# Optimization experiments

Measured on AMD Instinct MI355X. Metric: run time of the kernel, lower is better.

Reference implementation:

```python
import jax, jax.numpy as jnp
import numpy as np

V, BLOCK, L, H, C = 50257, 1024, 4, 12, 768
HS = C // H  # 64
EPS = 1e-6  # flax LayerNorm default


def _ln(x, scale, bias):
    mu = jnp.mean(x, axis=-1, keepdims=True)
    var = jnp.var(x, axis=-1, keepdims=True)
    return (x - mu) * jax.lax.rsqrt(var + EPS) * scale + bias


def setup_inputs() -> dict:
    key = jax.random.key(0)
    ks = jax.random.split(key, 12)
    B, T = 2, 1024
    inp = {
        'idx': jax.random.randint(ks[0], (B, T), 0, V),
        'targets': jax.random.randint(ks[1], (B, T), 0, V),
        'wte': jax.random.normal(ks[2], (V, C), jnp.float32) * 0.02,
        'wpe': jax.random.normal(ks[3], (BLOCK, C), jnp.float32) * 0.02,
        'ln1_s': jnp.ones((L, C), jnp.float32),
        'ln1_b': jnp.zeros((L, C), jnp.float32),
        'attn_k': jax.random.normal(ks[4], (L, C, H, 3 * HS), jnp.float32) * 0.02,
        'attn_b': jnp.zeros((L, H, 3 * HS), jnp.float32),
        'aproj_k': jax.random.normal(ks[5], (L, C, C), jnp.float32) * 0.02,
        'aproj_b': jnp.zeros((L, C), jnp.float32),
        'ln2_s': jnp.ones((L, C), jnp.float32),
        'ln2_b': jnp.zeros((L, C), jnp.float32),
        'fc_k': jax.random.normal(ks[6], (L, C, 4 * C), jnp.float32) * 0.02,
        'fc_b': jnp.zeros((L, 4 * C), jnp.float32),
        'mproj_k': jax.random.normal(ks[7], (L, 4 * C, C), jnp.float32) * 0.02,
        'mproj_b': jnp.zeros((L, C), jnp.float32),
        'lnf_s': jnp.ones((C,), jnp.float32),
        'lnf_b': jnp.zeros((C,), jnp.float32),
    }
    return inp


def _block(x, ln1_s, ln1_b, Wqkv, bqkv, Wo, bo, ln2_s, ln2_b, Wfc, bfc, Wmp, bmp, mask):
    B, T, _ = x.shape
    h = _ln(x, ln1_s, ln1_b)
    qkv = jnp.einsum('btc,chd->bhtd', h, Wqkv) + bqkv[:, None, :]  # [B,H,T,3HS]
    q, k, v = jnp.split(qkv, 3, axis=-1)
    att = jnp.einsum('bhtd,bhsd->bhts', q, k) * (1.0 / jnp.sqrt(jnp.float32(HS)))
    att = jnp.where(mask, att, -jnp.inf)
    att = jax.nn.softmax(att, axis=-1)
    y = jnp.einsum('bhts,bhsd->bthd', att, v).reshape(B, T, C)
    x = x + y @ Wo + bo
    h = _ln(x, ln2_s, ln2_b)
    h = jax.nn.gelu(h @ Wfc + bfc, approximate=True)
    x = x + h @ Wmp + bmp
    return x


def reference(idx, targets, wte, wpe, ln1_s, ln1_b, attn_k, attn_b, aproj_k, aproj_b,
              ln2_s, ln2_b, fc_k, fc_b, mproj_k, mproj_b, lnf_s, lnf_b):
    B, T = idx.shape
    x = wte[idx] + wpe[jnp.arange(T)][None]  # [B,T,C]
    mask = jnp.tril(jnp.ones((T, T), bool))[None, None]
    for l in range(L):
        x = _block(x, ln1_s[l], ln1_b[l], attn_k[l], attn_b[l], aproj_k[l], aproj_b[l],
                   ln2_s[l], ln2_b[l], fc_k[l], fc_b[l], mproj_k[l], mproj_b[l], mask)
    x = _ln(x, lnf_s, lnf_b)
    logits = jnp.einsum('btc,vc->btv', x, wte)  # tied output projection (wte.attend)
    logp = jax.nn.log_softmax(logits, axis=-1)
    loss = -jnp.mean(jnp.take_along_axis(logp, targets[..., None], axis=-1))
    return logits, loss
```

## Files before the change

kernel.cpp:

```cpp
#include <hip/hip_runtime.h>
#include <hip/hip_bf16.h>
#include <math.h>

typedef __attribute__((ext_vector_type(8))) short bf16x8;
typedef __attribute__((ext_vector_type(4))) float f32x4;

static constexpr int Bv   = 2;
static constexpr int Tv   = 1024;
static constexpr int Cv   = 768;
static constexpr int Hv   = 12;
static constexpr int Lv   = 4;
static constexpr int Vv   = 50257;
static constexpr int Mv   = 2048;
static constexpr int NT2  = 197;
static constexpr float EPSv = 1e-6f;

__device__ __forceinline__ void gload16(const void* g, void* l) {
    __builtin_amdgcn_global_load_lds((const __attribute__((address_space(1))) void*)g,
                                     (__attribute__((address_space(3))) void*)l, 16, 0, 0);
}
template<int N>
__device__ __forceinline__ void waitvm_barrier() {
    if constexpr (N == 0)      asm volatile("s_waitcnt vmcnt(0)\ns_barrier" ::: "memory");
    else if constexpr (N == 2) asm volatile("s_waitcnt vmcnt(2)\ns_barrier" ::: "memory");
    else if constexpr (N == 3) asm volatile("s_waitcnt vmcnt(3)\ns_barrier" ::: "memory");
    else if constexpr (N == 4) asm volatile("s_waitcnt vmcnt(4)\ns_barrier" ::: "memory");
    else if constexpr (N == 6) asm volatile("s_waitcnt vmcnt(6)\ns_barrier" ::: "memory");
    else                       asm volatile("s_waitcnt vmcnt(8)\ns_barrier" ::: "memory");
}
__device__ __forceinline__ void lgkm0_barrier() {
    asm volatile("s_waitcnt lgkmcnt(0)\ns_barrier" ::: "memory");
}

__global__ void embed_kernel(const int* __restrict__ idx,
                             const float* __restrict__ wte,
                             const float* __restrict__ wpe,
                             float* __restrict__ x) {
    int row = blockIdx.x;
    int t   = row & (Tv - 1);
    int tok = idx[row];
    const float* src = wte + (size_t)tok * Cv;
    const float* pos = wpe + (size_t)t * Cv;
    float* dst = x + (size_t)row * Cv;
    for (int c = threadIdx.x; c < Cv; c += 256)
        dst[c] = src[c] + pos[c];
}

__device__ __forceinline__ ushort4 pack4bf(float4 v) {
    ushort4 u;
    u.x = __bfloat16_as_ushort(__float2bfloat16(v.x));
    u.y = __bfloat16_as_ushort(__float2bfloat16(v.y));
    u.z = __bfloat16_as_ushort(__float2bfloat16(v.z));
    u.w = __bfloat16_as_ushort(__float2bfloat16(v.w));
    return u;
}

__global__ void ln_kernel(const float* __restrict__ in,
                          const float* __restrict__ sc,
                          const float* __restrict__ bi,
                          __hip_bfloat16* __restrict__ out) {
    int row  = blockIdx.x * 4 + (threadIdx.x >> 6);
    int lane = threadIdx.x & 63;
    const float4* xr = (const float4*)(in + (size_t)row * Cv);
    float4 a = xr[lane], b = xr[lane + 64], c = xr[lane + 128];
    float sum = a.x + a.y + a.z + a.w + b.x + b.y + b.z + b.w + c.x + c.y + c.z + c.w;
    float sq  = a.x*a.x + a.y*a.y + a.z*a.z + a.w*a.w
              + b.x*b.x + b.y*b.y + b.z*b.z + b.w*b.w
              + c.x*c.x + c.y*c.y + c.z*c.z + c.w*c.w;
    #pragma unroll
    for (int off = 32; off; off >>= 1) {
        sum += __shfl_xor(sum, off, 64);
        sq  += __shfl_xor(sq,  off, 64);
    }
    float mean = sum * (1.0f / Cv);
    float var  = sq * (1.0f / Cv) - mean * mean;
    float rs   = rsqrtf(var + EPSv);
    const float4* s4 = (const float4*)sc;
    const float4* b4 = (const float4*)bi;
    ushort4* orow = (ushort4*)(out + (size_t)row * Cv);
    #pragma unroll
    for (int i = 0; i < 3; ++i) {
        float4 v = (i == 0) ? a : (i == 1) ? b : c;
        float4 s = s4[lane + 64 * i];
        float4 t = b4[lane + 64 * i];
        float4 o;
        o.x = (v.x - mean) * rs * s.x + t.x;
        o.y = (v.y - mean) * rs * s.y + t.y;
        o.z = (v.z - mean) * rs * s.z + t.z;
        o.w = (v.w - mean) * rs * s.w + t.w;
        orow[lane + 64 * i] = pack4bf(o);
    }
}

__global__ void wtrans_kernel(const float* __restrict__ in,
                              __hip_bfloat16* __restrict__ out, int K, int N,
                              size_t inLS, size_t outLS) {
    __shared__ float tile[32][33];
    in  += (size_t)blockIdx.z * inLS;
    out += (size_t)blockIdx.z * outLS;
    int k0 = blockIdx.y * 32, n0 = blockIdx.x * 32;
    int tx = threadIdx.x & 31, ty = threadIdx.x >> 5;
    #pragma unroll
    for (int i = 0; i < 4; ++i)
        tile[ty + i * 8][tx] = in[(size_t)(k0 + ty + i * 8) * N + n0 + tx];
    __syncthreads();
    #pragma unroll
    for (int i = 0; i < 4; ++i)
        out[(size_t)(n0 + ty + i * 8) * K + k0 + tx] =
            __float2bfloat16(tile[tx][ty + i * 8]);
}

__global__ void cvt_kernel(const float* __restrict__ in,
                           __hip_bfloat16* __restrict__ out, int n4) {
    int stride = gridDim.x * 256;
    for (int i = blockIdx.x * 256 + threadIdx.x; i < n4; i += stride) {
        float4 v = ((const float4*)in)[i];
        ((ushort4*)out)[i] = pack4bf(v);
    }
}

__global__ void vtrans_kernel(const __hip_bfloat16* __restrict__ qkv,
                              __hip_bfloat16* __restrict__ vt) {
    __shared__ __hip_bfloat16 tile[32][33];
    int bh = blockIdx.z;
    int b = bh / Hv, h = bh % Hv;
    int t0 = blockIdx.x * 32, d0 = blockIdx.y * 32;
    int tx = threadIdx.x & 31, ty = threadIdx.x >> 5;
    #pragma unroll
    for (int i = 0; i < 4; ++i)
        tile[ty + i * 8][tx] =
            qkv[(size_t)(b * Tv + t0 + ty + i * 8) * 2304 + h * 192 + 128 + d0 + tx];
    __syncthreads();
    #pragma unroll
    for (int i = 0; i < 4; ++i)
        vt[((size_t)bh * 64 + d0 + ty + i * 8) * Tv + t0 + tx] = tile[tx][ty + i * 8];
}

template<int EPI, int BM>
__launch_bounds__(256)
__global__ void gemm_bf16(const __hip_bfloat16* __restrict__ A,
                          const __hip_bfloat16* __restrict__ Bt,
                          const float* __restrict__ bias,
                          const float* R, float* Cf,
                          __hip_bfloat16* __restrict__ Cb,
                          int M, int N, int K) {
    constexpr int FM  = BM / 32;
    constexpr int NA  = BM / 64;
    constexpr int LPT = NA + 1;
    __shared__ __hip_bfloat16 As[3][BM * 32];
    __shared__ __hip_bfloat16 Bs[3][64 * 32];
    int tid = threadIdx.x;
    int wave = tid >> 6, lane = tid & 63;
    int wr = wave >> 1, wc = wave & 1;
    int rowBase = blockIdx.y * BM, colBase = blockIdx.x * 64;

    f32x4 acc[FM][2] = {};

    int srow  = wave * 16 + (lane >> 2);
    int skcol = (lane & 3) * 8;
    const __hip_bfloat16* Ap0 = A + (size_t)(rowBase + srow) * K + skcol;
    const __hip_bfloat16* Ap1 = (NA > 1) ? (Ap0 + (size_t)64 * K) : Ap0;
    const __hip_bfloat16* Bp0 = Bt + (size_t)(colBase + srow) * K + skcol;
    int ldso = wave * 512;

    int aoff = (wr * (BM / 2) + (lane & 15)) * 32 + (lane >> 4) * 8;
    int boff = (wc * 32 + (lane & 15)) * 32 + (lane >> 4) * 8;

    auto stage = [&](int buf) {
        gload16(Ap0, &As[buf][ldso]);
        if constexpr (NA > 1) gload16(Ap1, &As[buf][2048 + ldso]);
        gload16(Bp0, &Bs[buf][ldso]);
        Ap0 += 32;
        if constexpr (NA > 1) Ap1 += 32;
        Bp0 += 32;
    };

    stage(0); stage(1); stage(2);

    int nt = K / 32;
    int cur = 0;
    for (int t = 0; t < nt; ++t) {
        if (t < nt - 2)       waitvm_barrier<2 * LPT>();
        else if (t == nt - 2) waitvm_barrier<LPT>();
        else                  waitvm_barrier<0>();

        bf16x8 av[FM], bv[2];
        #pragma unroll
        for (int m = 0; m < FM; ++m) av[m] = *(const bf16x8*)&As[cur][aoff + m * 512];
        #pragma unroll
        for (int n = 0; n < 2; ++n)  bv[n] = *(const bf16x8*)&Bs[cur][boff + n * 512];
        lgkm0_barrier();

        if (t + 3 < nt) stage(cur);

        #pragma unroll
        for (int m = 0; m < FM; ++m)
            #pragma unroll
            for (int n = 0; n < 2; ++n)
                acc[m][n] = __builtin_amdgcn_mfma_f32_16x16x32_bf16(
                    av[m], bv[n], acc[m][n], 0, 0, 0);
        cur = (cur == 2) ? 0 : cur + 1;
    }

    int fq = lane >> 4, fr = lane & 15;
    #pragma unroll
    for (int m = 0; m < FM; ++m) {
        #pragma unroll
        for (int n = 0; n < 2; ++n) {
            f32x4 v = acc[m][n];
            int col = colBase + wc * 32 + n * 16 + fr;
            #pragma unroll
            for (int j = 0; j < 4; ++j) {
                int row = rowBase + wr * (BM / 2) + m * 16 + fq * 4 + j;
                float val = v[j] + bias[col];
                if (EPI == 1) {
                    val += R[(size_t)row * N + col];
                    Cf[(size_t)row * N + col] = val;
                } else {
                    if (EPI == 2) {
                        float u = val;
                        float cc = 0.7978845608028654f * (u + 0.044715f * u * u * u);
                        val = 0.5f * u * (1.0f + tanhf(cc));
                    }
                    Cb[(size_t)row * N + col] = __float2bfloat16(val);
                }
            }
        }
    }
}

__launch_bounds__(256)
__global__ void attn_kernel(const __hip_bfloat16* __restrict__ qkv,
                            const __hip_bfloat16* __restrict__ vt,
                            __hip_bfloat16* __restrict__ att) {
    __shared__ __hip_bfloat16 Qs[64 * 64];
    __shared__ __hip_bfloat16 Ks[64 * 64];
    __shared__ __hip_bfloat16 Vs[64 * 64];
    __shared__ __hip_bfloat16 Ps[64 * 64];
    int bh = blockIdx.x;
    int b = bh / Hv, h = bh % Hv;
    int qt = (int)gridDim.y - 1 - (int)blockIdx.y;
    int q0 = qt * 64;
    int tid = threadIdx.x, wave = tid >> 6, lane = tid & 63;
    int g = lane >> 4, fr = lane & 15;
    int srow8 = lane >> 3, sc8 = lane & 7;

    const __hip_bfloat16* qbase = qkv + (size_t)(b * Tv + q0) * 2304 + h * 192;
    #pragma unroll
    for (int i = 0; i < 2; ++i) {
        int row = wave * 16 + i * 8 + srow8;
        gload16(qbase + (size_t)row * 2304 + ((sc8 ^ (row & 7)) * 8),
                Qs + (wave * 16 + i * 8) * 64);
    }

    f32x4 accO[4] = {};
    float mrun[4] = {-1e30f, -1e30f, -1e30f, -1e30f};
    float lrun[4] = {0.f, 0.f, 0.f, 0.f};

    for (int kv = 0; kv <= qt; ++kv) {
        int s0 = kv * 64;
        __syncthreads();
        const __hip_bfloat16* kbase = qkv + (size_t)(b * Tv + s0) * 2304 + h * 192 + 64;
        const __hip_bfloat16* vbase = vt + (size_t)bh * 64 * Tv + s0;
        #pragma unroll
        for (int i = 0; i < 2; ++i) {
            int row = wave * 16 + i * 8 + srow8;
            gload16(kbase + (size_t)row * 2304 + ((sc8 ^ (row & 7)) * 8),
                    Ks + (wave * 16 + i * 8) * 64);
            gload16(vbase + (size_t)row * Tv + ((sc8 ^ (row & 7)) * 8),
                    Vs + (wave * 16 + i * 8) * 64);
        }
        __syncthreads();

        f32x4 s4[4] = {};
        #pragma unroll
        for (int kk = 0; kk < 2; ++kk) {
            int qrow = wave * 16 + fr;
            bf16x8 qa = *(const bf16x8*)&Qs[qrow * 64 + (((g + 4 * kk) ^ (fr & 7)) * 8)];
            #pragma unroll
            for (int n = 0; n < 4; ++n) {
                int krow = n * 16 + fr;
                bf16x8 kb = *(const bf16x8*)&Ks[krow * 64 + (((g + 4 * kk) ^ (fr & 7)) * 8)];
                s4[n] = __builtin_amdgcn_mfma_f32_16x16x32_bf16(qa, kb, s4[n], 0, 0, 0);
            }
        }

        bool dia = (kv == qt);
        #pragma unroll
        for (int j = 0; j < 4; ++j) {
            int qg = q0 + wave * 16 + g * 4 + j;
            float sj[4], mx = -1e30f;
            #pragma unroll
            for (int n = 0; n < 4; ++n) {
                float v = s4[n][j] * 0.125f;
                if (dia && (s0 + n * 16 + fr) > qg) v = -1e30f;
                sj[n] = v;
                mx = fmaxf(mx, v);
            }
            #pragma unroll
            for (int off = 1; off < 16; off <<= 1)
                mx = fmaxf(mx, __shfl_xor(mx, off, 64));
            float mnew = fmaxf(mrun[j], mx);
            float ps = 0.f;
            unsigned short pb[4];
            #pragma unroll
            for (int n = 0; n < 4; ++n) {
                float p = __expf(sj[n] - mnew);
                __hip_bfloat16 pc = __float2bfloat16(p);
                pb[n] = __bfloat16_as_ushort(pc);
                ps += __bfloat162float(pc);
            }
            #pragma unroll
            for (int off = 1; off < 16; off <<= 1)
                ps += __shfl_xor(ps, off, 64);
            float cr = __expf(mrun[j] - mnew);
            lrun[j] = lrun[j] * cr + ps;
            mrun[j] = mnew;
            int prow = wave * 16 + g * 4 + j;
            #pragma unroll
            for (int n = 0; n < 4; ++n) {
                int byteoff = (32 * n + 2 * fr) ^ ((prow & 7) << 4);
                ((unsigned short*)Ps)[prow * 64 + (byteoff >> 1)] = pb[n];
            }
            #pragma unroll
            for (int n = 0; n < 4; ++n) accO[n][j] *= cr;
        }
        __syncthreads();

        #pragma unroll
        for (int kk = 0; kk < 2; ++kk) {
            int prow = wave * 16 + fr;
            bf16x8 pa = *(const bf16x8*)&Ps[prow * 64 + (((g + 4 * kk) ^ (fr & 7)) * 8)];
            #pragma unroll
            for (int n = 0; n < 4; ++n) {
                int vrow = n * 16 + fr;
                bf16x8 vb = *(const bf16x8*)&Vs[vrow * 64 + (((g + 4 * kk) ^ (fr & 7)) * 8)];
                accO[n] = __builtin_amdgcn_mfma_f32_16x16x32_bf16(pa, vb, accO[n], 0, 0, 0);
            }
        }
    }

    #pragma unroll
    for (int j = 0; j < 4; ++j) {
        float inv = 1.0f / lrun[j];
        int row = b * Tv + q0 + wave * 16 + g * 4 + j;
        #pragma unroll
        for (int n = 0; n < 4; ++n)
            att[(size_t)row * Cv + h * 64 + n * 16 + fr] =
                __float2bfloat16(accO[n][j] * inv);
    }
}

__launch_bounds__(512, 1)
__global__ void lmhead_kernel(const __hip_bfloat16* __restrict__ A,
                              const __hip_bfloat16* __restrict__ Bt,
                              float* __restrict__ Cf,
                              float* __restrict__ pLse) {
    constexpr int K = Cv, N = Vv;
    constexpr int nt = K / 64;
    __shared__ __hip_bfloat16 As[2][16384];
    __shared__ __hip_bfloat16 Bs[2][16384];
    __shared__ float ps[4][256];

    int bid = blockIdx.x;
    int nid = (bid & 7) * NT2 + (bid >> 3);
    int rowT = nid & 7, colT = nid >> 3;
    int rowBase = rowT * 256, colBase = colT * 256;

    int tid = threadIdx.x;
    int wv = tid >> 6, lane = tid & 63;
    int wr = wv >> 2, wc = wv & 3;
    int fq = lane >> 4, fr = lane & 15;
    int fr7 = fr & 7;

    f32x4 acc[8][4] = {};

    int r8 = lane >> 3;
    int cOff = ((lane & 7) ^ r8) * 8;
    const __hip_bfloat16* ApS[4];
    const __hip_bfloat16* BpS[4];
    #pragma unroll
    for (int i = 0; i < 4; ++i) {
        int rit = wv * 32 + i * 8 + r8;
        ApS[i] = A + (size_t)(rowBase + rit) * K + cOff;
        int rb = colBase + rit;
        if (rb >= N) rb = N - 1;
        BpS[i] = Bt + (size_t)rb * K + cOff;
    }

    auto stage = [&](int buf, int tile) {
        int k0 = tile * 64;
        #pragma unroll
        for (int i = 0; i < 4; ++i)
            gload16(ApS[i] + k0, &As[buf][(wv * 4 + i) * 512]);
        #pragma unroll
        for (int i = 0; i < 4; ++i)
            gload16(BpS[i] + k0, &Bs[buf][(wv * 4 + i) * 512]);
    };

    stage(0, 0);
    stage(1, 1);
    waitvm_barrier<8>();

    for (int t = 0; t < nt; ++t) {
        int cur = t & 1;
        const __hip_bfloat16* Ab = &As[cur][0];
        const __hip_bfloat16* Bb = &Bs[cur][0];

        bf16x8 av0[8], bv0[4];
        #pragma unroll
        for (int m = 0; m < 8; ++m)
            av0[m] = *(const bf16x8*)&Ab[(wr * 128 + m * 16 + fr) * 64 + ((fq ^ fr7) * 8)];
        #pragma unroll
        for (int n = 0; n < 4; ++n)
            bv0[n] = *(const bf16x8*)&Bb[(wc * 64 + n * 16 + fr) * 64 + ((fq ^ fr7) * 8)];
        __builtin_amdgcn_s_setprio(1);
        #pragma unroll
        for (int m = 0; m < 8; ++m)
            #pragma unroll
            for (int n = 0; n < 4; ++n)
                acc[m][n] = __builtin_amdgcn_mfma_f32_16x16x32_bf16(
                    av0[m], bv0[n], acc[m][n], 0, 0, 0);
        __builtin_amdgcn_s_setprio(0);

        bf16x8 av1[8], bv1[4];
        #pragma unroll
        for (int m = 0; m < 8; ++m)
            av1[m] = *(const bf16x8*)&Ab[(wr * 128 + m * 16 + fr) * 64 + (((4 + fq) ^ fr7) * 8)];
        #pragma unroll
        for (int n = 0; n < 4; ++n)
            bv1[n] = *(const bf16x8*)&Bb[(wc * 64 + n * 16 + fr) * 64 + (((4 + fq) ^ fr7) * 8)];
        lgkm0_barrier();

        if (t + 2 < nt) stage(cur, t + 2);

        __builtin_amdgcn_s_setprio(1);
        #pragma unroll
        for (int m = 0; m < 8; ++m)
            #pragma unroll
            for (int n = 0; n < 4; ++n)
                acc[m][n] = __builtin_amdgcn_mfma_f32_16x16x32_bf16(
                    av1[m], bv1[n], acc[m][n], 0, 0, 0);
        __builtin_amdgcn_s_setprio(0);

        if (t + 2 < nt) waitvm_barrier<8>();
        else            waitvm_barrier<0>();
    }

    #pragma unroll
    for (int m = 0; m < 8; ++m) {
        #pragma unroll
        for (int j = 0; j < 4; ++j) {
            int row = rowBase + wr * 128 + m * 16 + fq * 4 + j;
            float s = 0.f;
            #pragma unroll
            for (int n = 0; n < 4; ++n) {
                int col = colBase + wc * 64 + n * 16 + fr;
                float v = acc[m][n][j];
                if (col < N) {
                    Cf[(size_t)row * N + col] = v;
                    s += __expf(v);
                }
            }
            #pragma unroll
            for (int off = 1; off < 16; off <<= 1)
                s += __shfl_xor(s, off, 64);
            if (fr == 0)
                ps[wc][wr * 128 + m * 16 + fq * 4 + j] = s;
        }
    }
    __syncthreads();
    if (tid < 256)
        pLse[(size_t)(rowBase + tid) * NT2 + colT] =
            ps[0][tid] + ps[1][tid] + ps[2][tid] + ps[3][tid];
}

__global__ void plse_reduce_kernel(const float* __restrict__ pLse,
                                   const float* __restrict__ logits,
                                   const int* __restrict__ targets,
                                   float* __restrict__ rloss) {
    int row  = blockIdx.x * 4 + (threadIdx.x >> 6);
    int lane = threadIdx.x & 63;
    const float* pr = pLse + (size_t)row * NT2;
    float l = 0.f;
    for (int i = lane; i < NT2; i += 64) l += pr[i];
    #pragma unroll
    for (int off = 32; off; off >>= 1) l += __shfl_xor(l, off, 64);
    if (lane == 0)
        rloss[row] = logf(l) - logits[(size_t)row * Vv + targets[row]];
}

__global__ void loss_final_kernel(const float* __restrict__ rloss,
                                  float* __restrict__ out, int out_size) {
    float s = 0.f;
    for (int i = threadIdx.x; i < Mv; i += 256) s += rloss[i];
    #pragma unroll
    for (int off = 32; off; off >>= 1) s += __shfl_xor(s, off, 64);
    __shared__ float sw[4];
    int wave = threadIdx.x >> 6, lane = threadIdx.x & 63;
    if (lane == 0) sw[wave] = s;
    __syncthreads();
    if (threadIdx.x == 0)
        out[out_size - 1] = (sw[0] + sw[1] + sw[2] + sw[3]) / (float)Mv;
}

extern "C" void kernel_launch(void* const* d_in, const int* in_sizes, int n_in,
                              void* d_out, int out_size, void* d_ws, size_t ws_size,
                              hipStream_t stream) {
    const int*   idx     = (const int*)  d_in[0];
    const int*   targets = (const int*)  d_in[1];
    const float* wte     = (const float*)d_in[2];
    const float* wpe     = (const float*)d_in[3];
    const float* ln1_s   = (const float*)d_in[4];
    const float* ln1_b   = (const float*)d_in[5];
    const float* attn_k  = (const float*)d_in[6];
    const float* attn_b  = (const float*)d_in[7];
    const float* aproj_k = (const float*)d_in[8];
    const float* aproj_b = (const float*)d_in[9];
    const float* ln2_s   = (const float*)d_in[10];
    const float* ln2_b   = (const float*)d_in[11];
    const float* fc_k    = (const float*)d_in[12];
    const float* fc_b    = (const float*)d_in[13];
    const float* mproj_k = (const float*)d_in[14];
    const float* mproj_b = (const float*)d_in[15];
    const float* lnf_s   = (const float*)d_in[16];
    const float* lnf_b   = (const float*)d_in[17];

    float* out = (float*)d_out;
    char* ws  = (char*)d_ws;
    char* ob  = (char*)d_out;

    constexpr size_t NEED = 81962496ULL;
    if (ws_size < NEED) return;

    __hip_bfloat16* wte_bf = (__hip_bfloat16*)(ws + 0);
    __hip_bfloat16* h_bf   = (__hip_bfloat16*)(ws + 77194752);
    float*          pLse   = (float*)(ws + 80340480);
    float*          rloss  = (float*)(ws + 81954304);

    float*          x      = (float*)(ob + 0);
    __hip_bfloat16* qkv_bf = (__hip_bfloat16*)(ob + 6291456);
    __hip_bfloat16* vt_bf  = (__hip_bfloat16*)(ob + 15728640);
    __hip_bfloat16* att_bf = (__hip_bfloat16*)(ob + 18874368);
    __hip_bfloat16* fco_bf = (__hip_bfloat16*)(ob + 22020096);
    __hip_bfloat16* w0     = (__hip_bfloat16*)(ob + 34603008);
    __hip_bfloat16* w1     = (__hip_bfloat16*)(ob + 48758784);
    __hip_bfloat16* w2     = (__hip_bfloat16*)(ob + 53477376);
    __hip_bfloat16* w3     = (__hip_bfloat16*)(ob + 72351744);

    embed_kernel<<<Mv, 256, 0, stream>>>(idx, wte, wpe, x);

    wtrans_kernel<<<dim3(72, 24, 4), 256, 0, stream>>>(
        attn_k, w0, Cv, 2304, (size_t)Cv * 2304, (size_t)2304 * Cv);
    wtrans_kernel<<<dim3(24, 24, 4), 256, 0, stream>>>(
        aproj_k, w1, Cv, Cv, (size_t)Cv * Cv, (size_t)Cv * Cv);
    wtrans_kernel<<<dim3(96, 24, 4), 256, 0, stream>>>(
        fc_k, w2, Cv, 3072, (size_t)Cv * 3072, (size_t)3072 * Cv);
    wtrans_kernel<<<dim3(24, 96, 4), 256, 0, stream>>>(
        mproj_k, w3, 3072, Cv, (size_t)3072 * Cv, (size_t)Cv * 3072);

    for (int l = 0; l < Lv; ++l) {
        ln_kernel<<<512, 256, 0, stream>>>(x, ln1_s + l * Cv, ln1_b + l * Cv, h_bf);
        gemm_bf16<0, 128><<<dim3(36, 16), 256, 0, stream>>>(
            h_bf, w0 + (size_t)l * 2304 * Cv, attn_b + l * 2304, nullptr, nullptr,
            qkv_bf, Mv, 2304, Cv);
        vtrans_kernel<<<dim3(32, 2, 24), 256, 0, stream>>>(qkv_bf, vt_bf);
        attn_kernel<<<dim3(24, 16), 256, 0, stream>>>(qkv_bf, vt_bf, att_bf);
        gemm_bf16<1, 64><<<dim3(12, 32), 256, 0, stream>>>(
            att_bf, w1 + (size_t)l * Cv * Cv, aproj_b + l * Cv, x, x, nullptr,
            Mv, Cv, Cv);
        ln_kernel<<<512, 256, 0, stream>>>(x, ln2_s + l * Cv, ln2_b + l * Cv, h_bf);
        gemm_bf16<2, 128><<<dim3(48, 16), 256, 0, stream>>>(
            h_bf, w2 + (size_t)l * 3072 * Cv, fc_b + l * 3072, nullptr, nullptr,
            fco_bf, Mv, 3072, Cv);
        gemm_bf16<1, 64><<<dim3(12, 32), 256, 0, stream>>>(
            fco_bf, w3 + (size_t)l * Cv * 3072, mproj_b + l * Cv, x, x, nullptr,
            Mv, Cv, 3072);
    }

    ln_kernel<<<512, 256, 0, stream>>>(x, lnf_s, lnf_b, h_bf);
    cvt_kernel<<<2048, 256, 0, stream>>>(wte, wte_bf, (Vv * Cv) / 4);
    lmhead_kernel<<<8 * NT2, 512, 0, stream>>>(h_bf, wte_bf, out, pLse);
    plse_reduce_kernel<<<512, 256, 0, stream>>>(pLse, out, targets, rloss);
    loss_final_kernel<<<1, 256, 0, stream>>>(rloss, out, out_size);
}
```

Baseline: 942.1 us.

## Fuse V transpose into QKV GEMM epilogue and merge small launches

The QKV GEMM blocks that produce V now transpose their tile through LDS and write it straight into the vt buffer, replacing the separate vtrans kernel. The four weight-transpose launches are merged into one flat-grid kernel. The final loss reduction kernel is replaced by per-block atomicAdd into a slot zeroed inside cvt_kernel. This cuts launch count and one pass over V, but makes the loss summation order nondeterministic and skips writing V into qkv_bf.

Result: no change. 931.1 us (-1.2%).

```diff
diff --git a/kernel.cpp b/kernel.cpp
--- a/kernel.cpp
+++ b/kernel.cpp
@@ -92,13 +92,23 @@
     }
 }
 
-__global__ void wtrans_kernel(const float* __restrict__ in,
-                              __hip_bfloat16* __restrict__ out, int K, int N,
-                              size_t inLS, size_t outLS) {
+__global__ void wtrans_all_kernel(const float* __restrict__ a0, __hip_bfloat16* __restrict__ o0,
+                                  const float* __restrict__ a1, __hip_bfloat16* __restrict__ o1,
+                                  const float* __restrict__ a2, __hip_bfloat16* __restrict__ o2,
+                                  const float* __restrict__ a3, __hip_bfloat16* __restrict__ o3) {
     __shared__ float tile[32][33];
-    in  += (size_t)blockIdx.z * inLS;
-    out += (size_t)blockIdx.z * outLS;
-    int k0 = blockIdx.y * 32, n0 = blockIdx.x * 32;
+    int bid = blockIdx.x;
+    const float* in; __hip_bfloat16* out; int K, N, t;
+    if (bid < 6912)       { int l = bid / 1728;          t = bid % 1728;
+        in = a0 + (size_t)l * 768 * 2304; out = o0 + (size_t)l * 2304 * 768; K = 768;  N = 2304; }
+    else if (bid < 9216)  { int r = bid - 6912;  int l = r / 576;  t = r % 576;
+        in = a1 + (size_t)l * 768 * 768;  out = o1 + (size_t)l * 768 * 768;  K = 768;  N = 768;  }
+    else if (bid < 18432) { int r = bid - 9216;  int l = r / 2304; t = r % 2304;
+        in = a2 + (size_t)l * 768 * 3072; out = o2 + (size_t)l * 3072 * 768; K = 768;  N = 3072; }
+    else                  { int r = bid - 18432; int l = r / 2304; t = r % 2304;
+        in = a3 + (size_t)l * 3072 * 768; out = o3 + (size_t)l * 768 * 3072; K = 3072; N = 768;  }
+    int nx = N / 32;
+    int n0 = (t % nx) * 32, k0 = (t / nx) * 32;
     int tx = threadIdx.x & 31, ty = threadIdx.x >> 5;
     #pragma unroll
     for (int i = 0; i < 4; ++i)
@@ -111,29 +121,14 @@
 }
 
 __global__ void cvt_kernel(const float* __restrict__ in,
-                           __hip_bfloat16* __restrict__ out, int n4) {
+                           __hip_bfloat16* __restrict__ out, int n4,
+                           float* __restrict__ lossSlot) {
+    if (blockIdx.x == 0 && threadIdx.x == 0) *lossSlot = 0.f;
     int stride = gridDim.x * 256;
     for (int i = blockIdx.x * 256 + threadIdx.x; i < n4; i += stride) {
         float4 v = ((const float4*)in)[i];
         ((ushort4*)out)[i] = pack4bf(v);
     }
-}
-
-__global__ void vtrans_kernel(const __hip_bfloat16* __restrict__ qkv,
-                              __hip_bfloat16* __restrict__ vt) {
-    __shared__ __hip_bfloat16 tile[32][33];
-    int bh = blockIdx.z;
-    int b = bh / Hv, h = bh % Hv;
-    int t0 = blockIdx.x * 32, d0 = blockIdx.y * 32;
-    int tx = threadIdx.x & 31, ty = threadIdx.x >> 5;
-    #pragma unroll
-    for (int i = 0; i < 4; ++i)
-        tile[ty + i * 8][tx] =
-            qkv[(size_t)(b * Tv + t0 + ty + i * 8) * 2304 + h * 192 + 128 + d0 + tx];
-    __syncthreads();
-    #pragma unroll
-    for (int i = 0; i < 4; ++i)
-        vt[((size_t)bh * 64 + d0 + ty + i * 8) * Tv + t0 + tx] = tile[tx][ty + i * 8];
 }
 
 template<int EPI, int BM>
@@ -143,6 +138,7 @@
                           const float* __restrict__ bias,
                           const float* R, float* Cf,
                           __hip_bfloat16* __restrict__ Cb,
+                          __hip_bfloat16* __restrict__ vt,
                           int M, int N, int K) {
     constexpr int FM  = BM / 32;
     constexpr int NA  = BM / 64;
@@ -203,6 +199,37 @@
     }
 
     int fq = lane >> 4, fr = lane & 15;
+
+    if (EPI == 0 && vt != nullptr && (blockIdx.x % 3) == 2) {
+        __hip_bfloat16 (*Ts)[132] = (__hip_bfloat16(*)[132])&As[0][0];
+        __syncthreads();
+        #pragma unroll
+        for (int m = 0; m < FM; ++m) {
+            #pragma unroll
+            for (int n = 0; n < 2; ++n) {
+                int dloc = wc * 32 + n * 16 + fr;
+                #pragma unroll
+                for (int j = 0; j < 4; ++j) {
+                    int tl = wr * (BM / 2) + m * 16 + fq * 4 + j;
+                    float val = acc[m][n][j] + bias[colBase + dloc];
+                    Ts[dloc][tl] = __float2bfloat16(val);
+                }
+            }
+        }
+        __syncthreads();
+        int h  = blockIdx.x / 3;
+        int b  = rowBase >> 10;
+        int bh = b * Hv + h;
+        int t0 = rowBase & 1023;
+        int d = tid >> 2, part = tid & 3;
+        const ushort4* src = (const ushort4*)&Ts[d][part * 32];
+        ushort4* dst = (ushort4*)((__hip_bfloat16*)vt +
+                       ((size_t)bh * 64 + d) * Tv + t0 + part * 32);
+        #pragma unroll
+        for (int i = 0; i < 8; ++i) dst[i] = src[i];
+        return;
+    }
+
     #pragma unroll
     for (int m = 0; m < FM; ++m) {
         #pragma unroll
@@ -478,30 +505,21 @@
 __global__ void plse_reduce_kernel(const float* __restrict__ pLse,
                                    const float* __restrict__ logits,
                                    const int* __restrict__ targets,
-                                   float* __restrict__ rloss) {
-    int row  = blockIdx.x * 4 + (threadIdx.x >> 6);
+                                   float* __restrict__ lossOut) {
+    int wave = threadIdx.x >> 6;
+    int row  = blockIdx.x * 4 + wave;
     int lane = threadIdx.x & 63;
     const float* pr = pLse + (size_t)row * NT2;
     float l = 0.f;
     for (int i = lane; i < NT2; i += 64) l += pr[i];
     #pragma unroll
     for (int off = 32; off; off >>= 1) l += __shfl_xor(l, off, 64);
+    __shared__ float sr[4];
     if (lane == 0)
-        rloss[row] = logf(l) - logits[(size_t)row * Vv + targets[row]];
-}
-
-__global__ void loss_final_kernel(const float* __restrict__ rloss,
-                                  float* __restrict__ out, int out_size) {
-    float s = 0.f;
-    for (int i = threadIdx.x; i < Mv; i += 256) s += rloss[i];
-    #pragma unroll
-    for (int off = 32; off; off >>= 1) s += __shfl_xor(s, off, 64);
-    __shared__ float sw[4];
-    int wave = threadIdx.x >> 6, lane = threadIdx.x & 63;
-    if (lane == 0) sw[wave] = s;
+        sr[wave] = logf(l) - logits[(size_t)row * Vv + targets[row]];
     __syncthreads();
     if (threadIdx.x == 0)
-        out[out_size - 1] = (sw[0] + sw[1] + sw[2] + sw[3]) / (float)Mv;
+        atomicAdd(lossOut, (sr[0] + sr[1] + sr[2] + sr[3]) * (1.0f / Mv));
 }
 
 extern "C" void kernel_launch(void* const* d_in, const int* in_sizes, int n_in,
@@ -536,7 +554,6 @@
     __hip_bfloat16* wte_bf = (__hip_bfloat16*)(ws + 0);
     __hip_bfloat16* h_bf   = (__hip_bfloat16*)(ws + 77194752);
     float*          pLse   = (float*)(ws + 80340480);
-    float*          rloss  = (float*)(ws + 81954304);
 
     float*          x      = (float*)(ob + 0);
     __hip_bfloat16* qkv_bf = (__hip_bfloat16*)(ob + 6291456);
@@ -548,39 +565,33 @@
     __hip_bfloat16* w2     = (__hip_bfloat16*)(ob + 53477376);
     __hip_bfloat16* w3     = (__hip_bfloat16*)(ob + 72351744);
 
+    float* lossSlot = out + (out_size - 1);
+
     embed_kernel<<<Mv, 256, 0, stream>>>(idx, wte, wpe, x);
 
-    wtrans_kernel<<<dim3(72, 24, 4), 256, 0, stream>>>(
-        attn_k, w0, Cv, 2304, (size_t)Cv * 2304, (size_t)2304 * Cv);
-    wtrans_kernel<<<dim3(24, 24, 4), 256, 0, stream>>>(
-        aproj_k, w1, Cv, Cv, (size_t)Cv * Cv, (size_t)Cv * Cv);
-    wtrans_kernel<<<dim3(96, 24, 4), 256, 0, stream>>>(
-        fc_k, w2, Cv, 3072, (size_t)Cv * 3072, (size_t)3072 * Cv);
-    wtrans_kernel<<<dim3(24, 96, 4), 256, 0, stream>>>(
-        mproj_k, w3, 3072, Cv, (size_t)3072 * Cv, (size_t)Cv * 3072);
+    wtrans_all_kernel<<<27648, 256, 0, stream>>>(
+        attn_k, w0, aproj_k, w1, fc_k, w2, mproj_k, w3);
 
     for (int l = 0; l < Lv; ++l) {
         ln_kernel<<<512, 256, 0, stream>>>(x, ln1_s + l * Cv, ln1_b + l * Cv, h_bf);
         gemm_bf16<0, 128><<<dim3(36, 16), 256, 0, stream>>>(
             h_bf, w0 + (size_t)l * 2304 * Cv, attn_b + l * 2304, nullptr, nullptr,
-            qkv_bf, Mv, 2304, Cv);
-        vtrans_kernel<<<dim3(32, 2, 24), 256, 0, stream>>>(qkv_bf, vt_bf);
+            qkv_bf, vt_bf, Mv, 2304, Cv);
         attn_kernel<<<dim3(24, 16), 256, 0, stream>>>(qkv_bf, vt_bf, att_bf);
         gemm_bf16<1, 64><<<dim3(12, 32), 256, 0, stream>>>(
             att_bf, w1 + (size_t)l * Cv * Cv, aproj_b + l * Cv, x, x, nullptr,
-            Mv, Cv, Cv);
+            nullptr, Mv, Cv, Cv);
         ln_kernel<<<512, 256, 0, stream>>>(x, ln2_s + l * Cv, ln2_b + l * Cv, h_bf);
         gemm_bf16<2, 128><<<dim3(48, 16), 256, 0, stream>>>(
             h_bf, w2 + (size_t)l * 3072 * Cv, fc_b + l * 3072, nullptr, nullptr,
-            fco_bf, Mv, 3072, Cv);
+            fco_bf, nullptr, Mv, 3072, Cv);
         gemm_bf16<1, 64><<<dim3(12, 32), 256, 0, stream>>>(
             fco_bf, w3 + (size_t)l * Cv * 3072, mproj_b + l * Cv, x, x, nullptr,
-            Mv, Cv, 3072);
+            nullptr, Mv, Cv, 3072);
     }
 
     ln_kernel<<<512, 256, 0, stream>>>(x, lnf_s, lnf_b, h_bf);
-    cvt_kernel<<<2048, 256, 0, stream>>>(wte, wte_bf, (Vv * Cv) / 4);
+    cvt_kernel<<<2048, 256, 0, stream>>>(wte, wte_bf, (Vv * Cv) / 4, lossSlot);
     lmhead_kernel<<<8 * NT2, 512, 0, stream>>>(h_bf, wte_bf, out, pLse);
-    plse_reduce_kernel<<<512, 256, 0, stream>>>(pLse, out, targets, rloss);
-    loss_final_kernel<<<1, 256, 0, stream>>>(rloss, out, out_size);
-}
+    plse_reduce_kernel<<<512, 256, 0, stream>>>(pLse, out, targets, lossSlot);
+}
```
